# Optimization experiments

Measured on AMD Instinct MI355X. Metric: run time of the kernel, lower is better.

## Reference

```python
import jax, jax.numpy as jnp
import numpy as np

E = 2    # non-shared soft experts (nb_soft_experts - nb_shared_experts)
NH = 8   # attention heads
EPS = 1e-6


def _rmsnorm(u, w):
    return u * jax.lax.rsqrt(jnp.mean(u * u, axis=-1, keepdims=True) + EPS) * w


def _rotate(u):
    # torch rotate_embeddings: pairs (x0, x1) -> (-x1, x0), interleaved layout
    p = u.reshape(*u.shape[:-1], -1, 2)[..., ::-1]
    p = p * jnp.array([-1.0, 1.0], dtype=u.dtype)
    return p.reshape(u.shape)


def _rope(u, L, hs):
    # pos = 10000 ** ((-2*arange(0,hs,2) - 1) / hs); rotary = cat(t@pos, t@pos)
    inv = 10000.0 ** ((-2.0 * jnp.arange(0, hs, 2) - 1.0) / hs)      # [hs//2]
    ang = jnp.arange(L)[:, None] * inv[None, :]                      # [L, hs//2]
    rot = jnp.concatenate([ang, ang], axis=-1).astype(u.dtype)       # [L, hs]
    return u * jnp.cos(rot) + _rotate(u) * jnp.sin(rot)


def setup_inputs() -> dict:
    key = jax.random.key(0)
    B, T, C = 2, 2048, 512
    ks = jax.random.split(key, 8)
    s = lambda k_, sh: jax.random.normal(k_, sh, jnp.float32) / np.float32(np.sqrt(sh[0]))
    return dict(
        x=jax.random.normal(ks[0], (B, T, C), jnp.float32),
        W_router=s(ks[1], (C,)),
        W_q=s(ks[2], (C, E * C)),
        W_kv=s(ks[3], (C, 2 * C)),
        W_proj=s(ks[4], (C, C)),
        ln_w=jnp.ones((C,), jnp.float32),
        W_gate=s(ks[5], (C, E)),
        W_pred=s(ks[6], (C,)),
        k=1024,
    )


def reference(x, W_router, W_q, W_kv, W_proj, ln_w, W_gate, W_pred, k):
    B, T, C = x.shape
    hs = C // NH
    # --- MoD router: top-k token selection (apply_top_k_selection) ---
    logits = x @ W_router                                # [B, T]
    vals, idx = jax.lax.top_k(logits, k)                 # [B, k]
    w = jax.nn.sigmoid(vals)
    order = jnp.argsort(idx, axis=1)                     # restore temporal order
    idx = jnp.take_along_axis(idx, order, axis=1)
    w = jnp.take_along_axis(w, order, axis=1)
    sel = jnp.take_along_axis(x, idx[..., None], axis=1)  # gather [B, k, C]
    # --- heavy causal attention branch: E soft-expert queries, shared KV ---
    q = (sel @ W_q).reshape(B, k, E, C).transpose(0, 2, 1, 3)   # [B,E,k,C]
    kk, vv = jnp.split(sel @ W_kv, 2, axis=-1)                  # [B,k,C] each
    q = _rmsnorm(q, ln_w)
    kk = _rmsnorm(kk, ln_w)
    q = q.reshape(B, E, k, NH, hs).transpose(0, 1, 3, 2, 4)     # [B,E,NH,k,hs]
    kk = kk.reshape(B, k, NH, hs).transpose(0, 2, 1, 3)         # [B,NH,k,hs]
    vv = vv.reshape(B, k, NH, hs).transpose(0, 2, 1, 3)
    q = _rope(q, k, hs)
    kk = _rope(kk, k, hs)
    att = jnp.einsum('behqd,bhkd->behqk', q, kk) / np.float32(np.sqrt(hs))
    causal = jnp.tril(jnp.ones((k, k), bool))
    att = jnp.where(causal, att, jnp.finfo(att.dtype).min)
    att = jax.nn.softmax(att, axis=-1)
    y = jnp.einsum('behqk,bhkd->behqd', att, vv)                # [B,E,NH,k,hs]
    y = y.transpose(0, 1, 3, 2, 4).reshape(B, E, k, C) @ W_proj # [B,E,k,C]
    # --- soft-expert combination, router-weight scaling ---
    gate = jax.nn.softmax(sel @ W_gate, axis=-1)                # [B,k,E]
    yc = jnp.einsum('bke,bekc->bkc', gate, y) * w[..., None]    # [B,k,C]
    # --- scatter routed tokens back onto residual stream ---
    out = x.at[jnp.arange(B)[:, None], idx].add(yc)
    # --- sampling predictor BCE loss (calculate_sampling_predictor_loss) ---
    pl = x @ W_pred                                             # [B,T] logits
    tgt = jnp.zeros((B, T), x.dtype).at[jnp.arange(B)[:, None], idx].set(1.0)
    loss = jnp.mean(jnp.maximum(pl, 0) - pl * tgt + jnp.log1p(jnp.exp(-jnp.abs(pl))))
    return out, loss
```

## Files before the change

kernel.cpp:

```cpp
#include <hip/hip_runtime.h>
#include <cstdint>


#define DI __device__ __forceinline__

typedef __bf16 bf16x8 __attribute__((ext_vector_type(8)));
typedef float  f32x4  __attribute__((ext_vector_type(4)));
typedef short  s16x4  __attribute__((ext_vector_type(4)));
typedef short  s16x8  __attribute__((ext_vector_type(8)));

DI uint16_t f2bf(float f) {
    union { float f; uint32_t u; } v; v.f = f;
    uint32_t u = v.u;
    uint32_t r = (u + 0x7FFFu + ((u >> 16) & 1u)) >> 16;
    return (uint16_t)r;
}
DI float bf2f(uint32_t lo16) {
    union { uint32_t u; float f; } v; v.u = lo16 << 16; return v.f;
}

DI f32x4 mfma16(bf16x8 a, bf16x8 b, f32x4 c) {
    return __builtin_amdgcn_mfma_f32_16x16x32_bf16(a, b, c, 0, 0, 0);
}
DI f32x4 mfma_k16(s16x4 a, s16x4 b, f32x4 c) {
    return __builtin_amdgcn_mfma_f32_16x16x16bf16_1k(a, b, c, 0, 0, 0);
}

constexpr size_t OFF_LOGITS = 0;
constexpr size_t OFF_PL     = OFF_LOGITS + 4096 * 4;
constexpr size_t OFF_MASK   = OFF_PL     + 4096 * 4;
constexpr size_t OFF_POSMAP = OFF_MASK   + 4096 * 4;
constexpr size_t OFF_IDX    = OFF_POSMAP + 4096 * 4;
constexpr size_t OFF_WSEL   = OFF_IDX    + 2048 * 4;
constexpr size_t OFF_GATE   = OFF_WSEL   + 2048 * 4;
constexpr size_t OFF_SELBF  = OFF_GATE   + 4096 * 4;
constexpr size_t OFF_WQKVT  = OFF_SELBF  + 2048 * 512 * 2;
constexpr size_t OFF_WPROJT = OFF_WQKVT  + 2048 * 512 * 2;
constexpr size_t OFF_QKVRAW = OFF_WPROJT + 512 * 512 * 2;
constexpr size_t OFF_QH     = OFF_QKVRAW + (size_t)2048 * 2048 * 4;
constexpr size_t OFF_KH     = OFF_QH     + (size_t)2097152 * 2;
constexpr size_t OFF_VT     = OFF_KH     + (size_t)1048576 * 2;
constexpr size_t OFF_YBF    = OFF_VT     + (size_t)1048576 * 2;

__global__ void k_router(const float* __restrict__ x, const float* __restrict__ wr,
                         const float* __restrict__ wp,
                         float* __restrict__ logits, float* __restrict__ pl) {
    int wid  = (blockIdx.x * blockDim.x + threadIdx.x) >> 6;
    int lane = threadIdx.x & 63;
    if (wid >= 4096) return;
    const float* xr = x + (size_t)wid * 512;
    double s = 0.0; float sp = 0.f;
#pragma unroll
    for (int j = 0; j < 8; j++) {
        int c = lane + 64 * j;
        float xv = xr[c];
        s  += (double)xv * (double)wr[c];
        sp += xv * wp[c];
    }
    for (int m = 1; m < 64; m <<= 1) { s += __shfl_xor(s, m); sp += __shfl_xor(sp, m); }
    if (lane == 0) { logits[wid] = (float)s; pl[wid] = sp; }
}

__global__ void k_rank(const float* __restrict__ logits, int* __restrict__ mask) {
    int wid  = (blockIdx.x * blockDim.x + threadIdx.x) >> 6;
    int lane = threadIdx.x & 63;
    if (wid >= 4096) return;
    int b = wid >> 11, t = wid & 2047;
    const float* lb = logits + b * 2048;
    float v = lb[t];
    int cnt = 0;
    for (int j = 0; j < 32; j++) {
        int tp = lane + 64 * j;
        float lv = lb[tp];
        bool pred = (lv > v) || (lv == v && tp < t);
        cnt += __popcll(__ballot(pred));
    }
    if (lane == 0) mask[wid] = (cnt < 1024) ? 1 : 0;
}

__global__ void k_select(const float* __restrict__ logits, const int* __restrict__ mask,
                         int* __restrict__ idx, float* __restrict__ wsel,
                         int* __restrict__ posmap) {
    __shared__ int wsum[16], woff[16];
    int b = blockIdx.x, tid = threadIdx.x, lane = tid & 63, w = tid >> 6;
    int t0 = tid * 2, t1 = tid * 2 + 1;
    int m0 = mask[b * 2048 + t0], m1 = mask[b * 2048 + t1];
    int s = m0 + m1;
    int sc = s;
    for (int off = 1; off < 64; off <<= 1) {
        int v = __shfl_up(sc, off);
        if (lane >= off) sc += v;
    }
    if (lane == 63) wsum[w] = sc;
    __syncthreads();
    if (tid < 16) {
        int acc = 0;
        for (int j = 0; j < tid; j++) acc += wsum[j];
        woff[tid] = acc;
    }
    __syncthreads();
    int excl = woff[w] + sc - s;
    int p0 = excl, p1 = excl + m0;
    if (m0) {
        idx[b * 1024 + p0] = t0;
        float v = logits[b * 2048 + t0];
        wsel[b * 1024 + p0] = 1.f / (1.f + __expf(-v));
    }
    posmap[b * 2048 + t0] = m0 ? p0 : -1;
    if (m1) {
        idx[b * 1024 + p1] = t1;
        float v = logits[b * 2048 + t1];
        wsel[b * 1024 + p1] = 1.f / (1.f + __expf(-v));
    }
    posmap[b * 2048 + t1] = m1 ? p1 : -1;
}

__global__ __launch_bounds__(256) void k_castw(const float* __restrict__ Wq,
                                               const float* __restrict__ Wkv,
                                               const float* __restrict__ Wp,
                                               uint16_t* __restrict__ Wqkvt,
                                               uint16_t* __restrict__ Wprojt,
                                               const float4* __restrict__ xsrc,
                                               float4* __restrict__ outdst) {
    __shared__ float tile[64][65];
    int blk = blockIdx.x, tid = threadIdx.x;
    if (blk >= 320) {
        int j = (blk - 320) * 256 + tid;
        outdst[j] = xsrc[j];
        return;
    }
    const float* src; uint16_t* dst; int n0, c0, ldn;
    if (blk < 256) {
        int tn = blk & 31, tc = blk >> 5;
        n0 = tn * 64; c0 = tc * 64; ldn = 1024;
        if (n0 < 1024) { src = Wq; } else { src = Wkv; n0 -= 1024; }
        dst = Wqkvt + (size_t)(tn * 64) * 512 + c0;
    } else {
        int j = blk - 256; int tn = j & 7, tc = j >> 3;
        n0 = tn * 64; c0 = tc * 64; ldn = 512;
        src = Wp; dst = Wprojt + (size_t)n0 * 512 + c0;
    }
    int nl = tid & 63, cb = tid >> 6;
#pragma unroll
    for (int p = 0; p < 16; p++) {
        int cl_ = p * 4 + cb;
        tile[cl_][nl] = src[(size_t)(c0 + cl_) * ldn + n0 + nl];
    }
    __syncthreads();
    int cp = tid & 31, nb = tid >> 5;
#pragma unroll
    for (int p = 0; p < 8; p++) {
        int nl2 = p * 8 + nb;
        uint32_t pk = (uint32_t)f2bf(tile[cp * 2][nl2]) |
                      ((uint32_t)f2bf(tile[cp * 2 + 1][nl2]) << 16);
        *(uint32_t*)&dst[(size_t)nl2 * 512 + cp * 2] = pk;
    }
}

__global__ void k_gather_gate(const float* __restrict__ x, const int* __restrict__ idx,
                              const float* __restrict__ Wg,
                              uint16_t* __restrict__ selbf, float* __restrict__ gate) {
    __shared__ float red0[4], red1[4];
    int blk = blockIdx.x; int b = blk >> 10;
    int tid = threadIdx.x, lane = tid & 63, w = tid >> 6;
    int t = idx[blk];
    const float* xr = x + ((size_t)b * 2048 + t) * 512;
    int c = tid * 2;
    float v0 = xr[c], v1 = xr[c + 1];
    uint32_t pk = (uint32_t)f2bf(v0) | ((uint32_t)f2bf(v1) << 16);
    ((uint32_t*)(selbf + (size_t)blk * 512))[tid] = pk;
    float g0 = v0 * Wg[c * 2]     + v1 * Wg[(c + 1) * 2];
    float g1 = v0 * Wg[c * 2 + 1] + v1 * Wg[(c + 1) * 2 + 1];
    for (int m = 1; m < 64; m <<= 1) { g0 += __shfl_xor(g0, m); g1 += __shfl_xor(g1, m); }
    if (lane == 0) { red0[w] = g0; red1[w] = g1; }
    __syncthreads();
    if (tid == 0) {
        float a = red0[0] + red0[1] + red0[2] + red0[3];
        float bq = red1[0] + red1[1] + red1[2] + red1[3];
        float mx = fmaxf(a, bq);
        float ea = __expf(a - mx), eb = __expf(bq - mx), s = ea + eb;
        gate[blk * 2] = ea / s; gate[blk * 2 + 1] = eb / s;
    }
}

__global__ __launch_bounds__(256) void k_gemm(const uint16_t* __restrict__ A,
                                              const uint16_t* __restrict__ Bt,
                                              float* __restrict__ Cc,
                                              int M, int N, int Kd) {
    __shared__ uint16_t As[128 * 40], Bs[128 * 40];
    int tid = threadIdx.x, lane = tid & 63, w = tid >> 6;
    int m0 = blockIdx.x * 128, n0 = blockIdx.y * 128;
    int wr = (w >> 1) * 64, wc = (w & 1) * 64;
    f32x4 acc[4][4];
#pragma unroll
    for (int mt = 0; mt < 4; mt++)
#pragma unroll
        for (int nt = 0; nt < 4; nt++)
#pragma unroll
            for (int r = 0; r < 4; r++) acc[mt][nt][r] = 0.f;
    int arow = tid >> 2, akg = tid & 3;
    int K8 = Kd >> 3;
    const bf16x8* A8 = (const bf16x8*)A;
    const bf16x8* B8 = (const bf16x8*)Bt;
    for (int ks = 0; ks < Kd; ks += 32) {
        __syncthreads();
        int kc = (ks >> 3) + akg;
        bf16x8 va0 = A8[(size_t)(m0 + arow) * K8 + kc];
        bf16x8 va1 = A8[(size_t)(m0 + arow + 64) * K8 + kc];
        bf16x8 vb0 = B8[(size_t)(n0 + arow) * K8 + kc];
        bf16x8 vb1 = B8[(size_t)(n0 + arow + 64) * K8 + kc];
        *(bf16x8*)&As[arow * 40 + akg * 8] = va0;
        *(bf16x8*)&As[(arow + 64) * 40 + akg * 8] = va1;
        *(bf16x8*)&Bs[arow * 40 + akg * 8] = vb0;
        *(bf16x8*)&Bs[(arow + 64) * 40 + akg * 8] = vb1;
        __syncthreads();
        bf16x8 af[4], bfr[4];
#pragma unroll
        for (int t = 0; t < 4; t++) {
            af[t]  = *(const bf16x8*)&As[(wr + t * 16 + (lane & 15)) * 40 + (lane >> 4) * 8];
            bfr[t] = *(const bf16x8*)&Bs[(wc + t * 16 + (lane & 15)) * 40 + (lane >> 4) * 8];
        }
#pragma unroll
        for (int mt = 0; mt < 4; mt++)
#pragma unroll
            for (int nt = 0; nt < 4; nt++)
                acc[mt][nt] = mfma16(af[mt], bfr[nt], acc[mt][nt]);
    }
    int r0 = (lane >> 4) * 4, cl = lane & 15;
#pragma unroll
    for (int mt = 0; mt < 4; mt++)
#pragma unroll
        for (int nt = 0; nt < 4; nt++)
#pragma unroll
            for (int r = 0; r < 4; r++) {
                int row = m0 + wr + mt * 16 + r0 + r;
                int col = n0 + wc + nt * 16 + cl;
                Cc[(size_t)row * N + col] = acc[mt][nt][r];
            }
}

__global__ void k_norm_rope(const float* __restrict__ qkv, const float* __restrict__ lnw,
                            uint16_t* __restrict__ Qh, uint16_t* __restrict__ Kh) {
    __shared__ float red[4];
    int blk = blockIdx.x; int b = blk >> 10, i = blk & 1023;
    int tid = threadIdx.x, lane = tid & 63, w = tid >> 6;
    const float* row = qkv + (size_t)blk * 2048;
    int c0 = tid * 2;
    int d0 = c0 & 63, head = c0 >> 6;
    int j0 = d0 & 31, j1 = (d0 + 1) & 31;
    const float LN1E4_64 = 0.14391156831212787f;
    float fi = (float)i;
    float ang0 = fi * __expf(-(float)(4 * j0 + 1) * LN1E4_64);
    float ang1 = fi * __expf(-(float)(4 * j1 + 1) * LN1E4_64);
    float c_0 = cosf(ang0), s_0 = sinf(ang0);
    float c_1 = cosf(ang1), s_1 = sinf(ang1);
    float g0 = lnw[c0], g1 = lnw[c0 + 1];
    for (int which = 0; which < 3; which++) {
        int off = which * 512;
        float u0 = row[off + c0], u1 = row[off + c0 + 1];
        float ss = u0 * u0 + u1 * u1;
        for (int m = 1; m < 64; m <<= 1) ss += __shfl_xor(ss, m);
        __syncthreads();
        if (lane == 0) red[w] = ss;
        __syncthreads();
        float tot = red[0] + red[1] + red[2] + red[3];
        float rinv = rsqrtf(tot * (1.0f / 512.0f) + 1e-6f);
        float n0 = u0 * rinv * g0, n1 = u1 * rinv * g1;
        float r0 = n0 * c_0 - n1 * s_0;
        float r1 = n1 * c_1 + n0 * s_1;
        if (which < 2) {
            uint32_t pk = (uint32_t)f2bf(r0) | ((uint32_t)f2bf(r1) << 16);
            uint16_t* dstp = Qh + ((size_t)((b * 2 + which) * 8 + head) * 1024 + i) * 64 + d0;
            *(uint32_t*)dstp = pk;
        } else {
            uint32_t pk = (uint32_t)f2bf(r0 * 0.125f) | ((uint32_t)f2bf(r1 * 0.125f) << 16);
            uint16_t* dstp = Kh + ((size_t)(b * 8 + head) * 1024 + i) * 64 + d0;
            *(uint32_t*)dstp = pk;
        }
    }
}

__global__ __launch_bounds__(256) void k_vt(const float* __restrict__ qkv,
                                            uint16_t* __restrict__ Vt) {
    __shared__ float tile[64][65];
    int bh = blockIdx.x >> 4, kt = blockIdx.x & 15;
    int b = bh >> 3, h = bh & 7;
    int tid = threadIdx.x;
    int r = tid >> 2, cg = tid & 3;
    const float* srow = qkv + ((size_t)(b * 1024 + kt * 64 + r)) * 2048 + 1536 + h * 64 + cg * 16;
#pragma unroll
    for (int p = 0; p < 4; p++) {
        float4 v = *(const float4*)(srow + p * 4);
        tile[r][cg * 16 + p * 4 + 0] = v.x;
        tile[r][cg * 16 + p * 4 + 1] = v.y;
        tile[r][cg * 16 + p * 4 + 2] = v.z;
        tile[r][cg * 16 + p * 4 + 3] = v.w;
    }
    __syncthreads();
    int d = tid >> 2, kg = tid & 3;
    int t4 = kg;
    uint16_t* drow = Vt + ((size_t)(bh * 64 + d)) * 1024 + kt * 64;
#pragma unroll
    for (int g = 0; g < 4; g++) {
        uint16_t pk[4];
#pragma unroll
        for (int j = 0; j < 4; j++) pk[j] = f2bf(tile[t4 * 16 + g * 4 + j][d]);
        *(uint2*)&drow[g * 16 + t4 * 4] = *(const uint2*)pk;
    }
}

__global__ __launch_bounds__(512, 2) void k_attn(const uint16_t* __restrict__ Qh,
                                                 const uint16_t* __restrict__ Kh,
                                                 const uint16_t* __restrict__ Vt,
                                                 uint16_t* __restrict__ ybf) {
    __shared__ float cb[3][2][64][17];
    int blk = blockIdx.x;
    int qt = 31 - (blk >> 5);
    int inst = blk & 31;
    int h = inst & 7, b = inst >> 4;
    int tid = threadIdx.x, lane = tid & 63, w = tid >> 6;
    int wq = w & 1, ws = w >> 1;
    int qw = qt * 32 + wq * 16;
    const uint16_t* Qb = Qh + ((size_t)inst * 1024 + qw) * 64;
    const uint16_t* Kb = Kh + (size_t)(b * 8 + h) * 1024 * 64;
    const uint16_t* Vb = Vt + (size_t)(b * 8 + h) * 64 * 1024;
    int cl = lane & 15, gp = lane >> 4;
    bf16x8 qf0 = *(const bf16x8*)&Qb[cl * 64 + gp * 8];
    bf16x8 qf1 = *(const bf16x8*)&Qb[cl * 64 + 32 + gp * 8];
    f32x4 o[4];
#pragma unroll
    for (int dt = 0; dt < 4; dt++)
#pragma unroll
        for (int r = 0; r < 4; r++) o[dt][r] = 0.f;
    float ls = 0.f;
    int qa = qw + cl;
    const float L2E = 1.44269504f;
    const float SH  = -11.5415603f;

    for (int jt = ws * 64; jt <= qw; jt += 256) {
        f32x4 sv[4];
#pragma unroll
        for (int t = 0; t < 4; t++)
#pragma unroll
            for (int r = 0; r < 4; r++) sv[t][r] = 0.f;
#pragma unroll
        for (int t = 0; t < 4; t++) {
            const uint16_t* kr = &Kb[(size_t)(jt + t * 16 + cl) * 64 + gp * 8];
            bf16x8 k0 = *(const bf16x8*)kr;
            bf16x8 k1 = *(const bf16x8*)(kr + 32);
            sv[t] = mfma16(k0, qf0, sv[t]);
            sv[t] = mfma16(k1, qf1, sv[t]);
        }
        s16x8 vv0[4], vv1[4];
#pragma unroll
        for (int dt = 0; dt < 4; dt++) {
            const uint16_t* vrow = &Vb[(size_t)(dt * 16 + cl) * 1024 + jt + gp * 16];
            vv0[dt] = *(const s16x8*)vrow;
            vv1[dt] = *(const s16x8*)(vrow + 8);
        }
        bool bnd = (jt + 63 > qw);
        s16x4 pb[4];
#pragma unroll
        for (int t = 0; t < 4; t++) {
            union { s16x4 s4; __bf16 bf[4]; } pu;
#pragma unroll
            for (int r = 0; r < 4; r++) {
                float p = exp2f(fmaf(sv[t][r], L2E, SH));
                if (bnd) {
                    int kv = jt + t * 16 + gp * 4 + r;
                    p = (kv <= qa) ? p : 0.f;
                }
                ls += p;
                pu.bf[r] = (__bf16)p;
            }
            pb[t] = pu.s4;
        }
#pragma unroll
        for (int dt = 0; dt < 4; dt++) {
            s16x4 a0 = __builtin_shufflevector(vv0[dt], vv0[dt], 0, 1, 2, 3);
            s16x4 a1 = __builtin_shufflevector(vv0[dt], vv0[dt], 4, 5, 6, 7);
            s16x4 a2 = __builtin_shufflevector(vv1[dt], vv1[dt], 0, 1, 2, 3);
            s16x4 a3 = __builtin_shufflevector(vv1[dt], vv1[dt], 4, 5, 6, 7);
            o[dt] = mfma_k16(a0, pb[0], o[dt]);
            o[dt] = mfma_k16(a1, pb[1], o[dt]);
            o[dt] = mfma_k16(a2, pb[2], o[dt]);
            o[dt] = mfma_k16(a3, pb[3], o[dt]);
        }
    }
    ls += __shfl_xor(ls, 16);
    ls += __shfl_xor(ls, 32);
    if (ws != 0) {
#pragma unroll
        for (int dt = 0; dt < 4; dt++)
#pragma unroll
            for (int r = 0; r < 4; r++) cb[ws - 1][wq][lane][dt * 4 + r] = o[dt][r];
        cb[ws - 1][wq][lane][16] = ls;
    }
    __syncthreads();
    if (ws == 0) {
        float lst = ls + cb[0][wq][lane][16] + cb[1][wq][lane][16] + cb[2][wq][lane][16];
        float inv = 1.f / lst;
        uint16_t* yb = ybf + ((size_t)((inst >> 3) * 1024 + qw)) * 512 + h * 64;
#pragma unroll
        for (int dt = 0; dt < 4; dt++) {
            uint16_t pk[4];
#pragma unroll
            for (int r = 0; r < 4; r++) {
                float v = o[dt][r] + cb[0][wq][lane][dt * 4 + r]
                                   + cb[1][wq][lane][dt * 4 + r]
                                   + cb[2][wq][lane][dt * 4 + r];
                pk[r] = f2bf(v * inv);
            }
            *(uint2*)&yb[(size_t)cl * 512 + dt * 16 + gp * 4] = *(const uint2*)pk;
        }
    }
}

__global__ __launch_bounds__(256) void k_projc(const uint16_t* __restrict__ ybf,
                                               const uint16_t* __restrict__ Wprojt,
                                               const int* __restrict__ idx,
                                               const float* __restrict__ wsel,
                                               const float* __restrict__ gate,
                                               float* __restrict__ out) {
    __shared__ uint16_t As0[64 * 40], As1[64 * 40], Bs[64 * 40];
    int pid = blockIdx.x;
    int b = pid >> 4, pos0 = (pid & 15) * 64;
    int n0 = blockIdx.y * 64;
    int tid = threadIdx.x, lane = tid & 63, w = tid >> 6;
    int cl = lane & 15, gp = lane >> 4;
    f32x4 acc0[4], acc1[4];
#pragma unroll
    for (int nt = 0; nt < 4; nt++)
#pragma unroll
        for (int r = 0; r < 4; r++) { acc0[nt][r] = 0.f; acc1[nt][r] = 0.f; }
    int arow = tid >> 2, akg = tid & 3;
    const bf16x8* A8 = (const bf16x8*)ybf;
    const bf16x8* B8 = (const bf16x8*)Wprojt;
    size_t rowe0 = (size_t)(b * 2) * 1024 + pos0 + arow;
    for (int ks = 0; ks < 512; ks += 32) {
        __syncthreads();
        int kc = (ks >> 3) + akg;
        bf16x8 va0 = A8[rowe0 * 64 + kc];
        bf16x8 va1 = A8[(rowe0 + 1024) * 64 + kc];
        bf16x8 vb  = B8[(size_t)(n0 + arow) * 64 + kc];
        *(bf16x8*)&As0[arow * 40 + akg * 8] = va0;
        *(bf16x8*)&As1[arow * 40 + akg * 8] = va1;
        *(bf16x8*)&Bs[arow * 40 + akg * 8]  = vb;
        __syncthreads();
        bf16x8 a0 = *(const bf16x8*)&As0[(w * 16 + cl) * 40 + gp * 8];
        bf16x8 a1 = *(const bf16x8*)&As1[(w * 16 + cl) * 40 + gp * 8];
#pragma unroll
        for (int nt = 0; nt < 4; nt++) {
            bf16x8 bfr = *(const bf16x8*)&Bs[(nt * 16 + cl) * 40 + gp * 8];
            acc0[nt] = mfma16(a0, bfr, acc0[nt]);
            acc1[nt] = mfma16(a1, bfr, acc1[nt]);
        }
    }
#pragma unroll
    for (int r = 0; r < 4; r++) {
        int pos = pos0 + w * 16 + gp * 4 + r;
        int bk = b * 1024 + pos;
        int t = idx[bk];
        float wv = wsel[bk], g0 = gate[bk * 2], g1 = gate[bk * 2 + 1];
        float* orow = out + ((size_t)(b * 2048 + t)) * 512;
#pragma unroll
        for (int nt = 0; nt < 4; nt++) {
            int col = n0 + nt * 16 + cl;
            orow[col] += wv * (g0 * acc0[nt][r] + g1 * acc1[nt][r]);
        }
    }
}

__global__ void k_loss(const float* __restrict__ pl, const int* __restrict__ mask,
                       float* __restrict__ outloss) {
    __shared__ float red[16];
    int tid = threadIdx.x;
    float s = 0.f;
#pragma unroll
    for (int j = 0; j < 4; j++) {
        int i = tid * 4 + j;
        float p = pl[i];
        float tgt = (float)mask[i];
        s += fmaxf(p, 0.f) - p * tgt + log1pf(__expf(-fabsf(p)));
    }
    for (int mm = 1; mm < 64; mm <<= 1) s += __shfl_xor(s, mm);
    int lane = tid & 63, w = tid >> 6;
    if (lane == 0) red[w] = s;
    __syncthreads();
    if (tid == 0) {
        float t = 0.f;
        for (int q = 0; q < 16; q++) t += red[q];
        outloss[0] = t * (1.0f / 4096.0f);
    }
}

extern "C" void kernel_launch(void* const* d_in, const int* in_sizes, int n_in,
                              void* d_out, int out_size, void* d_ws, size_t ws_size,
                              hipStream_t stream) {
    const float* x        = (const float*)d_in[0];
    const float* W_router = (const float*)d_in[1];
    const float* W_q      = (const float*)d_in[2];
    const float* W_kv     = (const float*)d_in[3];
    const float* W_proj   = (const float*)d_in[4];
    const float* ln_w     = (const float*)d_in[5];
    const float* W_gate   = (const float*)d_in[6];
    const float* W_pred   = (const float*)d_in[7];

    char* ws = (char*)d_ws;
    float*    logits = (float*)   (ws + OFF_LOGITS);
    float*    pl     = (float*)   (ws + OFF_PL);
    int*      mask   = (int*)     (ws + OFF_MASK);
    int*      posmap = (int*)     (ws + OFF_POSMAP);
    int*      idx    = (int*)     (ws + OFF_IDX);
    float*    wsel   = (float*)   (ws + OFF_WSEL);
    float*    gate   = (float*)   (ws + OFF_GATE);
    uint16_t* selbf  = (uint16_t*)(ws + OFF_SELBF);
    uint16_t* Wqkvt  = (uint16_t*)(ws + OFF_WQKVT);
    uint16_t* Wprojt = (uint16_t*)(ws + OFF_WPROJT);
    float*    qkvraw = (float*)   (ws + OFF_QKVRAW);
    uint16_t* Qh     = (uint16_t*)(ws + OFF_QH);
    uint16_t* Kh     = (uint16_t*)(ws + OFF_KH);
    uint16_t* Vt     = (uint16_t*)(ws + OFF_VT);
    uint16_t* ybf    = (uint16_t*)(ws + OFF_YBF);
    float*    out    = (float*)d_out;

    k_castw      <<<2368, 256, 0, stream>>>(W_q, W_kv, W_proj, Wqkvt, Wprojt,
                                            (const float4*)x, (float4*)out);
    k_router     <<<1024, 256, 0, stream>>>(x, W_router, W_pred, logits, pl);
    k_rank       <<<1024, 256, 0, stream>>>(logits, mask);
    k_select     <<<2, 1024, 0, stream>>>(logits, mask, idx, wsel, posmap);
    k_gather_gate<<<2048, 256, 0, stream>>>(x, idx, W_gate, selbf, gate);
    k_gemm       <<<dim3(16, 16), 256, 0, stream>>>(selbf, Wqkvt, qkvraw, 2048, 2048, 512);
    k_norm_rope  <<<2048, 256, 0, stream>>>(qkvraw, ln_w, Qh, Kh);
    k_vt         <<<256, 256, 0, stream>>>(qkvraw, Vt);
    k_attn       <<<1024, 512, 0, stream>>>(Qh, Kh, Vt, ybf);
    k_projc      <<<dim3(32, 8), 256, 0, stream>>>(ybf, Wprojt, idx, wsel, gate, out);
    k_loss       <<<1, 1024, 0, stream>>>(pl, mask, out + 2097152);
}
```

Measured before the change: 99.93 us.

## Fuse prep and norm/V-transpose kernels; use global_load_lds GEMM with smaller N tile

Merges the router dot products into the weight-cast/copy kernel and folds the V transpose into the norm/rope kernel, which removes two launches. The QKV GEMM now uses 128x64 tiles and loads tiles straight into LDS with global_load_lds, without padding. Projection writes out = x + delta directly instead of read-modify-write. The out copy of x is kept, so routed rows are written twice, and unpadded LDS rows may cause bank conflicts.

```diff
diff --git a/kernel.cpp b/kernel.cpp
--- a/kernel.cpp
+++ b/kernel.cpp
@@ -15,15 +15,17 @@
     uint32_t r = (u + 0x7FFFu + ((u >> 16) & 1u)) >> 16;
     return (uint16_t)r;
 }
-DI float bf2f(uint32_t lo16) {
-    union { uint32_t u; float f; } v; v.u = lo16 << 16; return v.f;
-}
 
 DI f32x4 mfma16(bf16x8 a, bf16x8 b, f32x4 c) {
     return __builtin_amdgcn_mfma_f32_16x16x32_bf16(a, b, c, 0, 0, 0);
 }
 DI f32x4 mfma_k16(s16x4 a, s16x4 b, f32x4 c) {
     return __builtin_amdgcn_mfma_f32_16x16x16bf16_1k(a, b, c, 0, 0, 0);
+}
+DI void gload16(const void* g, void* l) {
+    __builtin_amdgcn_global_load_lds(
+        (const __attribute__((address_space(1))) uint32_t*)g,
+        (__attribute__((address_space(3))) uint32_t*)l, 16, 0, 0);
 }
 
 constexpr size_t OFF_LOGITS = 0;
@@ -42,23 +44,68 @@
 constexpr size_t OFF_VT     = OFF_KH     + (size_t)1048576 * 2;
 constexpr size_t OFF_YBF    = OFF_VT     + (size_t)1048576 * 2;
 
-__global__ void k_router(const float* __restrict__ x, const float* __restrict__ wr,
-                         const float* __restrict__ wp,
-                         float* __restrict__ logits, float* __restrict__ pl) {
-    int wid  = (blockIdx.x * blockDim.x + threadIdx.x) >> 6;
-    int lane = threadIdx.x & 63;
-    if (wid >= 4096) return;
-    const float* xr = x + (size_t)wid * 512;
-    double s = 0.0; float sp = 0.f;
-#pragma unroll
-    for (int j = 0; j < 8; j++) {
-        int c = lane + 64 * j;
-        float xv = xr[c];
-        s  += (double)xv * (double)wr[c];
-        sp += xv * wp[c];
-    }
-    for (int m = 1; m < 64; m <<= 1) { s += __shfl_xor(s, m); sp += __shfl_xor(sp, m); }
-    if (lane == 0) { logits[wid] = (float)s; pl[wid] = sp; }
+__global__ __launch_bounds__(256) void k_prep(const float* __restrict__ Wq,
+                                              const float* __restrict__ Wkv,
+                                              const float* __restrict__ Wp,
+                                              uint16_t* __restrict__ Wqkvt,
+                                              uint16_t* __restrict__ Wprojt,
+                                              const float4* __restrict__ xsrc,
+                                              float4* __restrict__ outdst,
+                                              const float* __restrict__ x,
+                                              const float* __restrict__ wr,
+                                              const float* __restrict__ wp,
+                                              float* __restrict__ logits,
+                                              float* __restrict__ pl) {
+    __shared__ float tile[64][65];
+    int blk = blockIdx.x, tid = threadIdx.x;
+    if (blk >= 2368) {
+        int rblk = blk - 2368;
+        int wid  = rblk * 4 + (tid >> 6);
+        int lane = tid & 63;
+        const float* xr = x + (size_t)wid * 512;
+        double s = 0.0; float sp = 0.f;
+#pragma unroll
+        for (int j = 0; j < 8; j++) {
+            int c = lane + 64 * j;
+            float xv = xr[c];
+            s  += (double)xv * (double)wr[c];
+            sp += xv * wp[c];
+        }
+        for (int m = 1; m < 64; m <<= 1) { s += __shfl_xor(s, m); sp += __shfl_xor(sp, m); }
+        if (lane == 0) { logits[wid] = (float)s; pl[wid] = sp; }
+        return;
+    }
+    if (blk >= 320) {
+        int j = (blk - 320) * 256 + tid;
+        outdst[j] = xsrc[j];
+        return;
+    }
+    const float* src; uint16_t* dst; int n0, c0, ldn;
+    if (blk < 256) {
+        int tn = blk & 31, tc = blk >> 5;
+        n0 = tn * 64; c0 = tc * 64; ldn = 1024;
+        if (n0 < 1024) { src = Wq; } else { src = Wkv; n0 -= 1024; }
+        dst = Wqkvt + (size_t)(tn * 64) * 512 + c0;
+    } else {
+        int j = blk - 256; int tn = j & 7, tc = j >> 3;
+        n0 = tn * 64; c0 = tc * 64; ldn = 512;
+        src = Wp; dst = Wprojt + (size_t)n0 * 512 + c0;
+    }
+    int nl = tid & 63, cb = tid >> 6;
+#pragma unroll
+    for (int p = 0; p < 16; p++) {
+        int cl_ = p * 4 + cb;
+        tile[cl_][nl] = src[(size_t)(c0 + cl_) * ldn + n0 + nl];
+    }
+    __syncthreads();
+    int cp = tid & 31, nb = tid >> 5;
+#pragma unroll
+    for (int p = 0; p < 8; p++) {
+        int nl2 = p * 8 + nb;
+        uint32_t pk = (uint32_t)f2bf(tile[cp * 2][nl2]) |
+                      ((uint32_t)f2bf(tile[cp * 2 + 1][nl2]) << 16);
+        *(uint32_t*)&dst[(size_t)nl2 * 512 + cp * 2] = pk;
+    }
 }
 
 __global__ void k_rank(const float* __restrict__ logits, int* __restrict__ mask) {
@@ -113,48 +160,6 @@
         wsel[b * 1024 + p1] = 1.f / (1.f + __expf(-v));
     }
     posmap[b * 2048 + t1] = m1 ? p1 : -1;
-}
-
-__global__ __launch_bounds__(256) void k_castw(const float* __restrict__ Wq,
-                                               const float* __restrict__ Wkv,
-                                               const float* __restrict__ Wp,
-                                               uint16_t* __restrict__ Wqkvt,
-                                               uint16_t* __restrict__ Wprojt,
-                                               const float4* __restrict__ xsrc,
-                                               float4* __restrict__ outdst) {
-    __shared__ float tile[64][65];
-    int blk = blockIdx.x, tid = threadIdx.x;
-    if (blk >= 320) {
-        int j = (blk - 320) * 256 + tid;
-        outdst[j] = xsrc[j];
-        return;
-    }
-    const float* src; uint16_t* dst; int n0, c0, ldn;
-    if (blk < 256) {
-        int tn = blk & 31, tc = blk >> 5;
-        n0 = tn * 64; c0 = tc * 64; ldn = 1024;
-        if (n0 < 1024) { src = Wq; } else { src = Wkv; n0 -= 1024; }
-        dst = Wqkvt + (size_t)(tn * 64) * 512 + c0;
-    } else {
-        int j = blk - 256; int tn = j & 7, tc = j >> 3;
-        n0 = tn * 64; c0 = tc * 64; ldn = 512;
-        src = Wp; dst = Wprojt + (size_t)n0 * 512 + c0;
-    }
-    int nl = tid & 63, cb = tid >> 6;
-#pragma unroll
-    for (int p = 0; p < 16; p++) {
-        int cl_ = p * 4 + cb;
-        tile[cl_][nl] = src[(size_t)(c0 + cl_) * ldn + n0 + nl];
-    }
-    __syncthreads();
-    int cp = tid & 31, nb = tid >> 5;
-#pragma unroll
-    for (int p = 0; p < 8; p++) {
-        int nl2 = p * 8 + nb;
-        uint32_t pk = (uint32_t)f2bf(tile[cp * 2][nl2]) |
-                      ((uint32_t)f2bf(tile[cp * 2 + 1][nl2]) << 16);
-        *(uint32_t*)&dst[(size_t)nl2 * 512 + cp * 2] = pk;
-    }
 }
 
 __global__ void k_gather_gate(const float* __restrict__ x, const int* __restrict__ idx,
@@ -187,50 +192,46 @@
                                               const uint16_t* __restrict__ Bt,
                                               float* __restrict__ Cc,
                                               int M, int N, int Kd) {
-    __shared__ uint16_t As[128 * 40], Bs[128 * 40];
+    __shared__ uint16_t As[128 * 32];
+    __shared__ uint16_t Bs[64 * 32];
     int tid = threadIdx.x, lane = tid & 63, w = tid >> 6;
-    int m0 = blockIdx.x * 128, n0 = blockIdx.y * 128;
-    int wr = (w >> 1) * 64, wc = (w & 1) * 64;
-    f32x4 acc[4][4];
+    int m0 = blockIdx.x * 128, n0 = blockIdx.y * 64;
+    int wr = (w >> 1) * 64, wc = (w & 1) * 32;
+    int cl = lane & 15, gp = lane >> 4;
+    f32x4 acc[4][2];
 #pragma unroll
     for (int mt = 0; mt < 4; mt++)
 #pragma unroll
-        for (int nt = 0; nt < 4; nt++)
+        for (int nt = 0; nt < 2; nt++)
 #pragma unroll
             for (int r = 0; r < 4; r++) acc[mt][nt][r] = 0.f;
-    int arow = tid >> 2, akg = tid & 3;
-    int K8 = Kd >> 3;
-    const bf16x8* A8 = (const bf16x8*)A;
-    const bf16x8* B8 = (const bf16x8*)Bt;
+    int srow = lane >> 2, skc = (lane & 3) * 8;
     for (int ks = 0; ks < Kd; ks += 32) {
         __syncthreads();
-        int kc = (ks >> 3) + akg;
-        bf16x8 va0 = A8[(size_t)(m0 + arow) * K8 + kc];
-        bf16x8 va1 = A8[(size_t)(m0 + arow + 64) * K8 + kc];
-        bf16x8 vb0 = B8[(size_t)(n0 + arow) * K8 + kc];
-        bf16x8 vb1 = B8[(size_t)(n0 + arow + 64) * K8 + kc];
-        *(bf16x8*)&As[arow * 40 + akg * 8] = va0;
-        *(bf16x8*)&As[(arow + 64) * 40 + akg * 8] = va1;
-        *(bf16x8*)&Bs[arow * 40 + akg * 8] = vb0;
-        *(bf16x8*)&Bs[(arow + 64) * 40 + akg * 8] = vb1;
-        __syncthreads();
-        bf16x8 af[4], bfr[4];
-#pragma unroll
-        for (int t = 0; t < 4; t++) {
-            af[t]  = *(const bf16x8*)&As[(wr + t * 16 + (lane & 15)) * 40 + (lane >> 4) * 8];
-            bfr[t] = *(const bf16x8*)&Bs[(wc + t * 16 + (lane & 15)) * 40 + (lane >> 4) * 8];
-        }
+        const uint16_t* ga0 = A + (size_t)(m0 + w * 32 + srow) * Kd + ks + skc;
+        gload16(ga0, &As[(w * 32) * 32]);
+        gload16(ga0 + (size_t)16 * Kd, &As[(w * 32 + 16) * 32]);
+        const uint16_t* gb = Bt + (size_t)(n0 + w * 16 + srow) * Kd + ks + skc;
+        gload16(gb, &Bs[(w * 16) * 32]);
+        __syncthreads();
+        bf16x8 af[4], bfr[2];
+#pragma unroll
+        for (int t = 0; t < 4; t++)
+            af[t] = *(const bf16x8*)&As[(wr + t * 16 + cl) * 32 + gp * 8];
+#pragma unroll
+        for (int t = 0; t < 2; t++)
+            bfr[t] = *(const bf16x8*)&Bs[(wc + t * 16 + cl) * 32 + gp * 8];
 #pragma unroll
         for (int mt = 0; mt < 4; mt++)
 #pragma unroll
-            for (int nt = 0; nt < 4; nt++)
+            for (int nt = 0; nt < 2; nt++)
                 acc[mt][nt] = mfma16(af[mt], bfr[nt], acc[mt][nt]);
     }
-    int r0 = (lane >> 4) * 4, cl = lane & 15;
+    int r0 = gp * 4;
 #pragma unroll
     for (int mt = 0; mt < 4; mt++)
 #pragma unroll
-        for (int nt = 0; nt < 4; nt++)
+        for (int nt = 0; nt < 2; nt++)
 #pragma unroll
             for (int r = 0; r < 4; r++) {
                 int row = m0 + wr + mt * 16 + r0 + r;
@@ -239,11 +240,42 @@
             }
 }
 
-__global__ void k_norm_rope(const float* __restrict__ qkv, const float* __restrict__ lnw,
-                            uint16_t* __restrict__ Qh, uint16_t* __restrict__ Kh) {
-    __shared__ float red[4];
-    int blk = blockIdx.x; int b = blk >> 10, i = blk & 1023;
-    int tid = threadIdx.x, lane = tid & 63, w = tid >> 6;
+__global__ __launch_bounds__(256) void k_nrv(const float* __restrict__ qkv,
+                                             const float* __restrict__ lnw,
+                                             uint16_t* __restrict__ Qh,
+                                             uint16_t* __restrict__ Kh,
+                                             uint16_t* __restrict__ Vt) {
+    __shared__ float tile[64][65];
+    int blk = blockIdx.x, tid = threadIdx.x;
+    if (blk >= 2048) {
+        int v = blk - 2048;
+        int bh = v >> 4, kt = v & 15;
+        int b = bh >> 3, h = bh & 7;
+        int r = tid >> 2, cg = tid & 3;
+        const float* srow = qkv + ((size_t)(b * 1024 + kt * 64 + r)) * 2048 + 1536 + h * 64 + cg * 16;
+#pragma unroll
+        for (int p = 0; p < 4; p++) {
+            float4 vv = *(const float4*)(srow + p * 4);
+            tile[r][cg * 16 + p * 4 + 0] = vv.x;
+            tile[r][cg * 16 + p * 4 + 1] = vv.y;
+            tile[r][cg * 16 + p * 4 + 2] = vv.z;
+            tile[r][cg * 16 + p * 4 + 3] = vv.w;
+        }
+        __syncthreads();
+        int d = tid >> 2, t4 = tid & 3;
+        uint16_t* drow = Vt + ((size_t)(bh * 64 + d)) * 1024 + kt * 64;
+#pragma unroll
+        for (int g = 0; g < 4; g++) {
+            uint16_t pk[4];
+#pragma unroll
+            for (int j = 0; j < 4; j++) pk[j] = f2bf(tile[t4 * 16 + g * 4 + j][d]);
+            *(uint2*)&drow[g * 16 + t4 * 4] = *(const uint2*)pk;
+        }
+        return;
+    }
+    int b = blk >> 10, i = blk & 1023;
+    int lane = tid & 63, w = tid >> 6;
+    float* red = &tile[0][0];
     const float* row = qkv + (size_t)blk * 2048;
     int c0 = tid * 2;
     int d0 = c0 & 63, head = c0 >> 6;
@@ -277,35 +309,6 @@
             uint16_t* dstp = Kh + ((size_t)(b * 8 + head) * 1024 + i) * 64 + d0;
             *(uint32_t*)dstp = pk;
         }
-    }
-}
-
-__global__ __launch_bounds__(256) void k_vt(const float* __restrict__ qkv,
-                                            uint16_t* __restrict__ Vt) {
-    __shared__ float tile[64][65];
-    int bh = blockIdx.x >> 4, kt = blockIdx.x & 15;
-    int b = bh >> 3, h = bh & 7;
-    int tid = threadIdx.x;
-    int r = tid >> 2, cg = tid & 3;
-    const float* srow = qkv + ((size_t)(b * 1024 + kt * 64 + r)) * 2048 + 1536 + h * 64 + cg * 16;
-#pragma unroll
-    for (int p = 0; p < 4; p++) {
-        float4 v = *(const float4*)(srow + p * 4);
-        tile[r][cg * 16 + p * 4 + 0] = v.x;
-        tile[r][cg * 16 + p * 4 + 1] = v.y;
-        tile[r][cg * 16 + p * 4 + 2] = v.z;
-        tile[r][cg * 16 + p * 4 + 3] = v.w;
-    }
-    __syncthreads();
-    int d = tid >> 2, kg = tid & 3;
-    int t4 = kg;
-    uint16_t* drow = Vt + ((size_t)(bh * 64 + d)) * 1024 + kt * 64;
-#pragma unroll
-    for (int g = 0; g < 4; g++) {
-        uint16_t pk[4];
-#pragma unroll
-        for (int j = 0; j < 4; j++) pk[j] = f2bf(tile[t4 * 16 + g * 4 + j][d]);
-        *(uint2*)&drow[g * 16 + t4 * 4] = *(const uint2*)pk;
     }
 }
 
@@ -421,6 +424,7 @@
                                                const int* __restrict__ idx,
                                                const float* __restrict__ wsel,
                                                const float* __restrict__ gate,
+                                               const float* __restrict__ x,
                                                float* __restrict__ out) {
     __shared__ uint16_t As0[64 * 40], As1[64 * 40], Bs[64 * 40];
     int pid = blockIdx.x;
@@ -462,11 +466,12 @@
         int bk = b * 1024 + pos;
         int t = idx[bk];
         float wv = wsel[bk], g0 = gate[bk * 2], g1 = gate[bk * 2 + 1];
+        const float* xrow = x + ((size_t)(b * 2048 + t)) * 512;
         float* orow = out + ((size_t)(b * 2048 + t)) * 512;
 #pragma unroll
         for (int nt = 0; nt < 4; nt++) {
             int col = n0 + nt * 16 + cl;
-            orow[col] += wv * (g0 * acc0[nt][r] + g1 * acc1[nt][r]);
+            orow[col] = xrow[col] + wv * (g0 * acc0[nt][r] + g1 * acc1[nt][r]);
         }
     }
 }
@@ -524,16 +529,15 @@
     uint16_t* ybf    = (uint16_t*)(ws + OFF_YBF);
     float*    out    = (float*)d_out;
 
-    k_castw      <<<2368, 256, 0, stream>>>(W_q, W_kv, W_proj, Wqkvt, Wprojt,
-                                            (const float4*)x, (float4*)out);
-    k_router     <<<1024, 256, 0, stream>>>(x, W_router, W_pred, logits, pl);
+    k_prep       <<<3392, 256, 0, stream>>>(W_q, W_kv, W_proj, Wqkvt, Wprojt,
+                                            (const float4*)x, (float4*)out,
+                                            x, W_router, W_pred, logits, pl);
     k_rank       <<<1024, 256, 0, stream>>>(logits, mask);
     k_select     <<<2, 1024, 0, stream>>>(logits, mask, idx, wsel, posmap);
     k_gather_gate<<<2048, 256, 0, stream>>>(x, idx, W_gate, selbf, gate);
-    k_gemm       <<<dim3(16, 16), 256, 0, stream>>>(selbf, Wqkvt, qkvraw, 2048, 2048, 512);
-    k_norm_rope  <<<2048, 256, 0, stream>>>(qkvraw, ln_w, Qh, Kh);
-    k_vt         <<<256, 256, 0, stream>>>(qkvraw, Vt);
+    k_gemm       <<<dim3(16, 32), 256, 0, stream>>>(selbf, Wqkvt, qkvraw, 2048, 2048, 512);
+    k_nrv        <<<2304, 256, 0, stream>>>(qkvraw, ln_w, Qh, Kh, Vt);
     k_attn       <<<1024, 512, 0, stream>>>(Qh, Kh, Vt, ybf);
-    k_projc      <<<dim3(32, 8), 256, 0, stream>>>(ybf, Wprojt, idx, wsel, gate, out);
+    k_projc      <<<dim3(32, 8), 256, 0, stream>>>(ybf, Wprojt, idx, wsel, gate, x, out);
     k_loss       <<<1, 1024, 0, stream>>>(pl, mask, out + 2097152);
 }
```

New measurement: 91.71 us. 8.2% less time.
